# Kernel tuning notes

Hardware: AMD Instinct MI355X
Metric: run time of the kernel (lower is better)

The kernel has to match this reference:

```python
import jax, jax.numpy as jnp
import numpy as np

EPS = 1e-5

def _conv1x1(x, w, b):
    # x: [B,C,H,W], w: [O,C,1,1], b: [O]
    return jnp.einsum('oc,bchw->bohw', w[:, :, 0, 0], x) + b[None, :, None, None]

def _maxpool(x, s):
    return jax.lax.reduce_window(x, -jnp.inf, jax.lax.max,
                                 (1, 1, s, s), (1, 1, s, s), 'VALID')

def _sra(x, gw, gb, tw, tb, pw, pb, ww, wb, scale):
    # embedded-Gaussian non-local block with spatial sub-sampling on phi/g
    B, C, H, W = x.shape
    ic = gw.shape[0]
    g = _maxpool(_conv1x1(x, gw, gb), scale).reshape(B, ic, -1)    # [B,ic,n]
    phi = _maxpool(_conv1x1(x, pw, pb), scale).reshape(B, ic, -1)  # [B,ic,n]
    theta = _conv1x1(x, tw, tb).reshape(B, ic, -1)                 # [B,ic,N]
    f = jnp.einsum('bcn,bcm->bnm', theta, phi)                     # [B,N,n]
    a = jax.nn.softmax(f, axis=-1)
    y = jnp.einsum('bnm,bcm->bcn', a, g).reshape(B, ic, H, W)
    return _conv1x1(y, ww, wb) + x

def _conv_bn(x, w, gamma, beta, mean, var):
    y = jax.lax.conv_general_dilated(x, w, (1, 1), ((1, 1), (1, 1)),
                                     dimension_numbers=('NCHW', 'OIHW', 'NCHW'))
    inv = gamma / jnp.sqrt(var + EPS)
    return y * inv[None, :, None, None] + (beta - mean * inv)[None, :, None, None]

def setup_inputs() -> dict:
    key = jax.random.key(0)
    B, C = 4, 32
    sizes = [96, 48, 24]
    inp = {}
    ks = iter(jax.random.split(key, 64))
    for i, hw in enumerate(sizes):
        inp[f'fea1_{i}'] = jax.random.normal(next(ks), (B, C, hw, hw), jnp.float32)
        inp[f'fea2_{i}'] = jax.random.normal(next(ks), (B, C, hw, hw), jnp.float32)
    for lv in (1, 2, 3):
        for nm in ('g', 't', 'p'):
            inp[f'{nm}{lv}_w'] = jax.random.normal(next(ks), (C, 2 * C, 1, 1), jnp.float32) * 0.05
            inp[f'{nm}{lv}_b'] = jax.random.normal(next(ks), (C,), jnp.float32) * 0.05
        inp[f'w{lv}_w'] = jax.random.normal(next(ks), (2 * C, C, 1, 1), jnp.float32) * 0.05
        inp[f'w{lv}_b'] = jax.random.normal(next(ks), (2 * C,), jnp.float32) * 0.05
        inp[f'c{lv}_w'] = jax.random.normal(next(ks), (C, 2 * C, 3, 3), jnp.float32) * 0.05
        inp[f'bn{lv}_g'] = jax.random.uniform(next(ks), (C,), jnp.float32, 0.5, 1.5)
        inp[f'bn{lv}_b'] = jax.random.normal(next(ks), (C,), jnp.float32) * 0.05
        inp[f'bn{lv}_m'] = jax.random.normal(next(ks), (C,), jnp.float32) * 0.05
        inp[f'bn{lv}_v'] = jax.random.uniform(next(ks), (C,), jnp.float32, 0.5, 1.5)
    return inp

def reference(fea1_0, fea1_1, fea1_2, fea2_0, fea2_1, fea2_2,
              g1_w, g1_b, t1_w, t1_b, p1_w, p1_b, w1_w, w1_b, c1_w, bn1_g, bn1_b, bn1_m, bn1_v,
              g2_w, g2_b, t2_w, t2_b, p2_w, p2_b, w2_w, w2_b, c2_w, bn2_g, bn2_b, bn2_m, bn2_v,
              g3_w, g3_b, t3_w, t3_b, p3_w, p3_b, w3_w, w3_b, c3_w, bn3_g, bn3_b, bn3_m, bn3_v):
    x1 = jnp.concatenate([fea1_0, fea2_0], axis=1)
    x2 = jnp.concatenate([fea1_1, fea2_1], axis=1)
    x3 = jnp.concatenate([fea1_2, fea2_2], axis=1)
    z1 = _sra(x1, g1_w, g1_b, t1_w, t1_b, p1_w, p1_b, w1_w, w1_b, 2)
    z2 = _sra(x2, g2_w, g2_b, t2_w, t2_b, p2_w, p2_b, w2_w, w2_b, 4)
    z3 = _sra(x3, g3_w, g3_b, t3_w, t3_b, p3_w, p3_b, w3_w, w3_b, 8)
    out1 = _conv_bn(z1, c1_w, bn1_g, bn1_b, bn1_m, bn1_v)
    out2 = _conv_bn(z2, c2_w, bn2_g, bn2_b, bn2_m, bn2_v)
    out3 = _conv_bn(z3, c3_w, bn3_g, bn3_b, bn3_m, bn3_v)
    return (out1, out2, out3)
```

## Files before the change

kernel.cpp:

```cpp
#include <hip/hip_runtime.h>
#include <hip/hip_bf16.h>

typedef __hip_bfloat16 bf16;
typedef __attribute__((ext_vector_type(8))) short short8;
typedef __attribute__((ext_vector_type(4))) float floatx4;

__device__ __forceinline__ float b2f(bf16 v) { return __bfloat162float(v); }
__device__ __forceinline__ bf16 f2b(float v) { return __float2bfloat16(v); }
__device__ __forceinline__ float ldv(const void* p, size_t i, bool f32) {
    return f32 ? ((const float*)p)[i] : b2f(((const bf16*)p)[i]);
}
__device__ __forceinline__ float s2f(short s) {
    unsigned int u = ((unsigned int)(unsigned short)s) << 16;
    float f; __builtin_memcpy(&f, &u, 4); return f;
}
__device__ __forceinline__ short f2s(float f) {
    bf16 h = f2b(f); short s; __builtin_memcpy(&s, &h, 2); return s;
}
#define MFMA16(a, b, c) __builtin_amdgcn_mfma_f32_16x16x32_bf16(a, b, c, 0, 0, 0)

struct Ptrs { const void* p[45]; };

struct Lvl {
    const void *f1, *f2;
    const float *wtgp, *btgp, *wbf, *bfold;
    const bf16 *Wt, *Wc3;
    bf16 *th, *g, *p, *phi, *gt, *yp, *z;
    float* lp;
    int N, n, npad, split, W, s, wp, H, tX, BN;
    size_t outOff;
};

__global__ void k_detect(const void* x, int* flag) {
    __shared__ int cnt;
    if (threadIdx.x == 0) cnt = 0;
    __syncthreads();
    const unsigned short* us = (const unsigned short*)x;
    int local = 0;
    for (int i = threadIdx.x; i < 8192; i += 256) {
        unsigned e = us[2 * i] & 0x7F80u;
        if (e == 0x7F80u || e == 0u) local++;
    }
    atomicAdd(&cnt, local);
    __syncthreads();
    if (threadIdx.x == 0) flag[0] = (cnt >= 8) ? 1 : 0;
}

#define O_WTGP  0
#define O_BTGP  6144
#define O_WBF   6240
#define O_BFOLD 6304
#define O_WT    6336
#define O_WC3   7360
#define LVS     16576

__global__ void k_prep(Ptrs in, const int* flag, float* __restrict__ wsf)
{
    int lv = blockIdx.y;
    float* base = wsf + (size_t)lv * LVS;
    const int wb0 = 6 + 13 * lv;
    const void* gw  = in.p[wb0 + 0];
    const void* gb  = in.p[wb0 + 1];
    const void* tw  = in.p[wb0 + 2];
    const void* tb  = in.p[wb0 + 3];
    const void* pw  = in.p[wb0 + 4];
    const void* pb  = in.p[wb0 + 5];
    const void* ww  = in.p[wb0 + 6];
    const void* wb  = in.p[wb0 + 7];
    const void* cw  = in.p[wb0 + 8];
    const void* bng = in.p[wb0 + 9];
    const void* bnb = in.p[wb0 + 10];
    const void* bnm = in.p[wb0 + 11];
    const void* bnv = in.p[wb0 + 12];
    bool f32 = flag[0] != 0;
    int gid = blockIdx.x * 256 + threadIdx.x;
    int stride = gridDim.x * 256;

    float* wtgp = base + O_WTGP;
    float* btgp = base + O_BTGP;
    float* wbf = base + O_WBF;
    float* bfold = base + O_BFOLD;
    bf16* Wt = (bf16*)(base + O_WT);
    bf16* Wc3 = (bf16*)(base + O_WC3);

    for (int e = gid; e < 64 * 96; e += stride) {
        int k = e / 96, c = e % 96;
        float v;
        if (c < 32)      v = ldv(tw, (size_t)c * 64 + k, f32);
        else if (c < 64) v = ldv(gw, (size_t)(c - 32) * 64 + k, f32);
        else             v = ldv(pw, (size_t)(c - 64) * 64 + k, f32);
        wtgp[e] = v;
    }
    for (int e = gid; e < 96; e += stride) {
        float v = (e < 32) ? ldv(tb, e, f32)
                           : (e < 64 ? ldv(gb, e - 32, f32) : ldv(pb, e - 64, f32));
        btgp[e] = v;
    }
    for (int e = gid; e < 64 * 32; e += stride)
        Wt[e] = f2b(ldv(ww, e, f32));
    for (int e = gid; e < 64; e += stride) wbf[e] = ldv(wb, e, f32);
    for (int e = gid; e < 18432; e += stride) {
        int k = e & 31, n = (e >> 5) & 15, ot = (e >> 9) & 1;
        int tap = (e >> 10) % 9, cc = e / 9216;
        int o = ot * 16 + n, c = cc * 32 + k;
        float inv = ldv(bng, o, f32) * rsqrtf(ldv(bnv, o, f32) + 1e-5f);
        Wc3[e] = f2b(ldv(cw, ((size_t)o * 64 + c) * 9 + tap, f32) * inv);
    }
    for (int e = gid; e < 32; e += stride) {
        float inv = ldv(bng, e, f32) * rsqrtf(ldv(bnv, e, f32) + 1e-5f);
        bfold[e] = ldv(bnb, e, f32) - ldv(bnm, e, f32) * inv;
    }
}

__global__ void k_tgp(Lvl a0, Lvl a1, Lvl a2, int s1, int s2, const int* flag)
{
    bool f32 = flag[0] != 0;
    int bid = blockIdx.x;
    const Lvl P = bid < s1 ? a0 : (bid < s2 ? a1 : a2);
    int local = bid - (bid < s1 ? 0 : (bid < s2 ? s1 : s2));
    int nbp = P.BN >> 8;
    int grp = local / nbp;
    int pb = local - grp * nbp;
    bf16* dst = (grp == 0) ? P.th : ((grp == 1) ? P.g : P.p);
    int co = grp * 32;
    int gid = pb * 256 + threadIdx.x;
    int N = P.N;
    int b = gid / N;
    int ii = gid - b * N;
    float acc[32];
#pragma unroll
    for (int c = 0; c < 32; c++) acc[c] = P.btgp[co + c];
    size_t base = (size_t)b * 32 * N + ii;
    for (int k = 0; k < 32; k++) {
        float xv = ldv(P.f1, base + (size_t)k * N, f32);
        const float* w = P.wtgp + k * 96 + co;
#pragma unroll
        for (int c = 0; c < 32; c++) acc[c] += xv * w[c];
    }
    for (int k = 0; k < 32; k++) {
        float xv = ldv(P.f2, base + (size_t)k * N, f32);
        const float* w = P.wtgp + (k + 32) * 96 + co;
#pragma unroll
        for (int c = 0; c < 32; c++) acc[c] += xv * w[c];
    }
    bf16* dp = dst + (size_t)gid * 32;
#pragma unroll
    for (int c = 0; c < 32; c++) dp[c] = f2b(acc[c]);
}

__global__ void k_pool(Lvl a0, Lvl a1, Lvl a2, int s1, int s2)
{
    int bid = blockIdx.x;
    const Lvl P = bid < s1 ? a0 : (bid < s2 ? a1 : a2);
    int local = bid - (bid < s1 ? 0 : (bid < s2 ? s1 : s2));
    int gid = local * 256 + threadIdx.x;
    int npad = P.npad;
    if (gid >= 4 * npad * 32) return;
    int c = gid & 31;
    int j = (gid >> 5) % npad;
    int b = gid / (32 * npad);
    float mg = 0.f, mp = 0.f;
    if (j < P.n) {
        int py = j / P.wp, px = j - py * P.wp;
        const int N = P.N;
        mg = -INFINITY; mp = -INFINITY;
        for (int dy = 0; dy < P.s; dy++)
            for (int dx = 0; dx < P.s; dx++) {
                int idx = (py * P.s + dy) * P.W + px * P.s + dx;
                size_t bse = ((size_t)b * N + idx) * 32 + c;
                mg = fmaxf(mg, b2f(P.g[bse]));
                mp = fmaxf(mp, b2f(P.p[bse]));
            }
    }
    P.phi[((size_t)b * npad + j) * 32 + c] = f2b(mp);
    P.gt[((size_t)b * 32 + c) * npad + j] = f2b(mg);
}

__launch_bounds__(256)
__global__ void k_attn(Lvl a0, Lvl a1, Lvl a2, int s1, int s2)
{
    __shared__ __align__(16) bf16 Pt_s[4 * 1152];
    int bid = blockIdx.x;
    const Lvl P = bid < s1 ? a0 : (bid < s2 ? a1 : a2);
    int local = bid - (bid < s1 ? 0 : (bid < s2 ? s1 : s2));
    int rowblocks = P.BN >> 6;
    int c = local / rowblocks;
    int rb = local - c * rowblocks;

    int tid = threadIdx.x, lane = tid & 63, wv = tid >> 6;
    int quad = lane >> 4, col = lane & 15;
    bf16* Pt = Pt_s + wv * 1152;
    int row0 = rb * 64;
    int b = row0 / P.N;
    int npad = P.npad;

    short8 ta = *(const short8*)(P.th + (size_t)(row0 + wv * 16 + col) * 32 + quad * 8);
    const bf16* php = P.phi + (size_t)b * npad * 32 + (size_t)col * 32 + quad * 8;
    const bf16* gtp = P.gt + (size_t)b * 32 * npad + (size_t)col * npad + quad * 8;

    floatx4 y0 = {0.f, 0.f, 0.f, 0.f}, y1 = {0.f, 0.f, 0.f, 0.f};
    float lp4[4] = {0.f, 0.f, 0.f, 0.f};
    const floatx4 zc = {0.f, 0.f, 0.f, 0.f};

    int js = c ? P.split : 0;
    int je = c ? npad : P.split;
    for (int j0 = js; j0 < je; j0 += 64) {
        floatx4 s0 = MFMA16(ta, *(const short8*)(php + (size_t)(j0 +  0) * 32), zc);
        floatx4 s1 = MFMA16(ta, *(const short8*)(php + (size_t)(j0 + 16) * 32), zc);
        floatx4 s2 = MFMA16(ta, *(const short8*)(php + (size_t)(j0 + 32) * 32), zc);
        floatx4 s3 = MFMA16(ta, *(const short8*)(php + (size_t)(j0 + 48) * 32), zc);
#pragma unroll
        for (int r = 0; r < 4; r++) {
            float p0 = __expf(s0[r]), p1 = __expf(s1[r]);
            float p2 = __expf(s2[r]), p3 = __expf(s3[r]);
            lp4[r] += (p0 + p1) + (p2 + p3);
            bf16* pr = Pt + (quad * 4 + r) * 72;
            pr[ 0 + col] = f2b(p0);
            pr[16 + col] = f2b(p1);
            pr[32 + col] = f2b(p2);
            pr[48 + col] = f2b(p3);
        }
#pragma unroll
        for (int kc = 0; kc < 2; kc++) {
            short8 pa = *(const short8*)(Pt + col * 72 + kc * 32 + quad * 8);
            short8 g0 = *(const short8*)(gtp + j0 + kc * 32);
            short8 g1 = *(const short8*)(gtp + (size_t)16 * npad + j0 + kc * 32);
            y0 = MFMA16(pa, g0, y0);
            y1 = MFMA16(pa, g1, y1);
        }
    }

#pragma unroll
    for (int r = 0; r < 4; r++) {
        float v = lp4[r];
        v += __shfl_xor(v, 1); v += __shfl_xor(v, 2);
        v += __shfl_xor(v, 4); v += __shfl_xor(v, 8);
        int grow = row0 + wv * 16 + quad * 4 + r;
        size_t o = ((size_t)c * P.BN + grow) * 32;
        P.yp[o + col] = f2b(y0[r]);
        P.yp[o + 16 + col] = f2b(y1[r]);
        if (col == 0) P.lp[(size_t)c * P.BN + grow] = v;
    }
}

__launch_bounds__(256)
__global__ void k_merge(Lvl a0, Lvl a1, Lvl a2, int s1, int s2, const int* flag)
{
    bool f32 = flag[0] != 0;
    __shared__ __align__(16) float zb[64 * 65];
    int bid = blockIdx.x;
    const Lvl P = bid < s1 ? a0 : (bid < s2 ? a1 : a2);
    int rb = bid - (bid < s1 ? 0 : (bid < s2 ? s1 : s2));
    int tid = threadIdx.x, lane = tid & 63, wv = tid >> 6;
    int quad = lane >> 4, col = lane & 15;
    int row0 = rb * 64;
    int b = row0 / P.N;
    int pix0 = row0 - b * P.N;

    int grow = row0 + wv * 16 + col;
    short8 v0 = *(const short8*)(P.yp + (size_t)grow * 32 + quad * 8);
    short8 v1 = *(const short8*)(P.yp + ((size_t)P.BN + grow) * 32 + quad * 8);
    float L = P.lp[grow] + P.lp[(size_t)P.BN + grow] - (float)(P.npad - P.n);
    float invL = 1.f / L;
    short8 ya;
#pragma unroll
    for (int j = 0; j < 8; j++)
        ya[j] = f2s((s2f(v0[j]) + s2f(v1[j])) * invL);

    const floatx4 zc = {0.f, 0.f, 0.f, 0.f};
    floatx4 zt[4];
#pragma unroll
    for (int ot = 0; ot < 4; ot++) {
        short8 wbv = *(const short8*)(P.Wt + (size_t)(ot * 16 + col) * 32 + quad * 8);
        zt[ot] = MFMA16(ya, wbv, zc);
    }
#pragma unroll
    for (int ot = 0; ot < 4; ot++)
#pragma unroll
        for (int r = 0; r < 4; r++)
            zb[(wv * 16 + quad * 4 + r) * 65 + ot * 16 + col] = zt[ot][r];
    __syncthreads();

    const void* fx = (wv < 2) ? P.f1 : P.f2;
#pragma unroll
    for (int k = 0; k < 16; k++) {
        int o = wv * 16 + k, op = o & 31;
        float a = zb[lane * 65 + o] + P.wbf[o];
        a += ldv(fx, (size_t)(b * 32 + op) * P.N + pix0 + lane, f32);
        P.z[((size_t)(b * 64 + o)) * P.N + pix0 + lane] = f2b(a);
    }
}

__launch_bounds__(256)
__global__ void k_conv3m(Lvl a0, Lvl a1, Lvl a2, int s1, int s2,
                         void* out, const int* flag)
{
    bool f32 = flag[0] != 0;
    __shared__ __align__(16) bf16 zh[324 * 34];
    int bid = blockIdx.x;
    const Lvl P = bid < s1 ? a0 : (bid < s2 ? a1 : a2);
    int local = bid - (bid < s1 ? 0 : (bid < s2 ? s1 : s2));
    const int H = P.H, W = H, Npix = H * W, tX = P.tX;
    int tid = threadIdx.x, lane = tid & 63, wv = tid >> 6;
    int quad = lane >> 4, col = lane & 15;
    int tpi = tX * tX;
    int b = local / tpi;
    int t = local - b * tpi;
    int ty = t / tX, tx = t - ty * tX;
    int y0 = ty * 16, x0 = tx * 16;

    floatx4 acc[4][2];
#pragma unroll
    for (int pt = 0; pt < 4; pt++)
#pragma unroll
        for (int ot = 0; ot < 2; ot++) acc[pt][ot] = (floatx4){0.f, 0.f, 0.f, 0.f};

    for (int cc = 0; cc < 2; cc++) {
        __syncthreads();
        for (int e = tid; e < 324 * 32; e += 256) {
            int c = e / 324, pix = e - c * 324;
            int hy = pix / 18, hx = pix - hy * 18;
            int gy = y0 - 1 + hy, gx = x0 - 1 + hx;
            bf16 v = f2b(0.f);
            if (gy >= 0 && gy < H && gx >= 0 && gx < W)
                v = P.z[((size_t)(b * 64 + cc * 32 + c)) * Npix + gy * W + gx];
            zh[pix * 34 + c] = v;
        }
        __syncthreads();
        short8 Bf[9][2];
        const bf16* wp = P.Wc3 + (size_t)cc * 9216 + col * 32 + quad * 8;
#pragma unroll
        for (int tap = 0; tap < 9; tap++)
#pragma unroll
            for (int ot = 0; ot < 2; ot++)
                Bf[tap][ot] = *(const short8*)(wp + (tap * 2 + ot) * 512);
#pragma unroll
        for (int pt = 0; pt < 4; pt++) {
            int yy = wv * 4 + pt;
#pragma unroll
            for (int tap = 0; tap < 9; tap++) {
                int dy = tap / 3, dx = tap - dy * 3;
                short8 A = *(const short8*)(zh + ((yy + dy) * 18 + (col + dx)) * 34 + quad * 8);
                acc[pt][0] = MFMA16(A, Bf[tap][0], acc[pt][0]);
                acc[pt][1] = MFMA16(A, Bf[tap][1], acc[pt][1]);
            }
        }
    }
#pragma unroll
    for (int pt = 0; pt < 4; pt++) {
        int oy = y0 + wv * 4 + pt;
        if (oy >= H) continue;
#pragma unroll
        for (int ot = 0; ot < 2; ot++) {
            int o = ot * 16 + col;
            size_t ob = P.outOff + (size_t)(b * 32 + o) * Npix + (size_t)oy * W;
            float bias = P.bfold[o];
#pragma unroll
            for (int r = 0; r < 4; r++) {
                int ox = x0 + quad * 4 + r;
                if (ox >= W) continue;
                float a = acc[pt][ot][r] + bias;
                if (f32) ((float*)out)[ob + ox] = a;
                else     ((bf16*)out)[ob + ox] = f2b(a);
            }
        }
    }
}

extern "C" void kernel_launch(void* const* d_in, const int* in_sizes, int n_in,
                              void* d_out, int out_size, void* d_ws, size_t ws_size,
                              hipStream_t stream)
{
    const int Hs[3] = {96, 48, 24};
    const int ss[3] = {2, 4, 8};
    const int npads[3] = {2304, 192, 64};
    const int splits[3] = {1152, 128, 64};
    const size_t outOff[3] = {0, 1179648, 1474560};

    int* flag = (int*)d_ws;
    float* wsf = (float*)d_ws + 16;
    float* lpbase = wsf + 3 * LVS;
    bf16* bb = (bf16*)(lpbase + 96768);

    const size_t o_gp[3] = {0, 2359296, 2949120};
    const size_t R_TH = 3096576;
    const size_t o_th[3] = {R_TH, R_TH + 1179648, R_TH + 1474560};
    const size_t R_PHI = 4644864;
    const size_t o_phi[3] = {R_PHI, R_PHI + 294912, R_PHI + 319488};
    const size_t R_GT = 4972544;
    const size_t o_gt[3] = {R_GT, R_GT + 294912, R_GT + 319488};
    const size_t o_z[3] = {R_TH, R_TH + 2359296, R_TH + 2949120};
    const size_t o_lp[3] = {0, 73728, 92160};

    k_detect<<<1, 256, 0, stream>>>(d_in[0], flag);

    Ptrs hp;
    for (int i = 0; i < 45 && i < n_in; i++) hp.p[i] = d_in[i];
    k_prep<<<dim3(8, 3), 256, 0, stream>>>(hp, flag, wsf);

    Lvl L[3];
    for (int lv = 0; lv < 3; lv++) {
        int H = Hs[lv], N = H * H;
        float* base = wsf + (size_t)lv * LVS;
        L[lv].f1 = d_in[2 * lv];
        L[lv].f2 = d_in[2 * lv + 1];
        L[lv].wtgp = base + O_WTGP;
        L[lv].btgp = base + O_BTGP;
        L[lv].wbf = base + O_WBF;
        L[lv].bfold = base + O_BFOLD;
        L[lv].Wt = (const bf16*)(base + O_WT);
        L[lv].Wc3 = (const bf16*)(base + O_WC3);
        L[lv].th = bb + o_th[lv];
        L[lv].g = bb + o_gp[lv];
        L[lv].p = bb + o_gp[lv] + (size_t)4 * N * 32;
        L[lv].phi = bb + o_phi[lv];
        L[lv].gt = bb + o_gt[lv];
        L[lv].yp = bb + o_gp[lv];
        L[lv].z = bb + o_z[lv];
        L[lv].lp = lpbase + o_lp[lv];
        L[lv].N = N;
        L[lv].n = (H / ss[lv]) * (H / ss[lv]);
        L[lv].npad = npads[lv];
        L[lv].split = splits[lv];
        L[lv].W = H;
        L[lv].s = ss[lv];
        L[lv].wp = H / ss[lv];
        L[lv].H = H;
        L[lv].tX = (H + 15) / 16;
        L[lv].BN = 4 * N;
        L[lv].outOff = outOff[lv];
    }

    k_tgp<<<567, 256, 0, stream>>>(L[0], L[1], L[2], 432, 540, flag);
    k_pool<<<1280, 256, 0, stream>>>(L[0], L[1], L[2], 1152, 1248);
    k_attn<<<1512, 256, 0, stream>>>(L[0], L[1], L[2], 1152, 1440);
    k_merge<<<756, 256, 0, stream>>>(L[0], L[1], L[2], 576, 720, flag);
    k_conv3m<<<196, 256, 0, stream>>>(L[0], L[1], L[2], 144, 180, d_out, flag);
}
```

Baseline: 320.0 us.

## Generalize attention key split to configurable chunks with register prefetch and double-buffered LDS

Replaces the fixed two-way split of the softmax key dimension with a per-level chunk count (up to four for the largest level when the workspace is large enough), launching more attention blocks. The merge kernel sums the partial numerators and denominators across all chunks. Inside the attention loop, the phi and g tiles for the next iteration are prefetched into registers and the P tile alternates between two LDS buffers to overlap loads with MFMA work. The workspace layout is reorganised to hold the larger partial buffers, at the cost of more LDS, more registers per thread and more partial-result traffic.

```diff
diff --git a/kernel.cpp b/kernel.cpp
--- a/kernel.cpp
+++ b/kernel.cpp
@@ -27,7 +27,7 @@
     const bf16 *Wt, *Wc3;
     bf16 *th, *g, *p, *phi, *gt, *yp, *z;
     float* lp;
-    int N, n, npad, split, W, s, wp, H, tX, BN;
+    int N, n, npad, nch, W, s, wp, H, tX, BN;
     size_t outOff;
 };
 
@@ -179,7 +179,7 @@
 __launch_bounds__(256)
 __global__ void k_attn(Lvl a0, Lvl a1, Lvl a2, int s1, int s2)
 {
-    __shared__ __align__(16) bf16 Pt_s[4 * 1152];
+    __shared__ __align__(16) bf16 Pt_s[8 * 1152];
     int bid = blockIdx.x;
     const Lvl P = bid < s1 ? a0 : (bid < s2 ? a1 : a2);
     int local = bid - (bid < s1 ? 0 : (bid < s2 ? s1 : s2));
@@ -189,11 +189,15 @@
 
     int tid = threadIdx.x, lane = tid & 63, wv = tid >> 6;
     int quad = lane >> 4, col = lane & 15;
-    bf16* Pt = Pt_s + wv * 1152;
+    bf16* Pt0 = Pt_s + wv * 2304;
     int row0 = rb * 64;
     int b = row0 / P.N;
     int npad = P.npad;
 
+    int T = npad >> 6, C = P.nch;
+    int js = ((T * c) / C) << 6;
+    int je = ((T * (c + 1)) / C) << 6;
+
     short8 ta = *(const short8*)(P.th + (size_t)(row0 + wv * 16 + col) * 32 + quad * 8);
     const bf16* php = P.phi + (size_t)b * npad * 32 + (size_t)col * 32 + quad * 8;
     const bf16* gtp = P.gt + (size_t)b * 32 * npad + (size_t)col * npad + quad * 8;
@@ -202,19 +206,37 @@
     float lp4[4] = {0.f, 0.f, 0.f, 0.f};
     const floatx4 zc = {0.f, 0.f, 0.f, 0.f};
 
-    int js = c ? P.split : 0;
-    int je = c ? npad : P.split;
+    short8 ph[4], gg[4];
+#pragma unroll
+    for (int k = 0; k < 4; k++)
+        ph[k] = *(const short8*)(php + (size_t)(js + 16 * k) * 32);
+    gg[0] = *(const short8*)(gtp + js);
+    gg[1] = *(const short8*)(gtp + js + 32);
+    gg[2] = *(const short8*)(gtp + (size_t)16 * npad + js);
+    gg[3] = *(const short8*)(gtp + (size_t)16 * npad + js + 32);
+
     for (int j0 = js; j0 < je; j0 += 64) {
-        floatx4 s0 = MFMA16(ta, *(const short8*)(php + (size_t)(j0 +  0) * 32), zc);
-        floatx4 s1 = MFMA16(ta, *(const short8*)(php + (size_t)(j0 + 16) * 32), zc);
-        floatx4 s2 = MFMA16(ta, *(const short8*)(php + (size_t)(j0 + 32) * 32), zc);
-        floatx4 s3 = MFMA16(ta, *(const short8*)(php + (size_t)(j0 + 48) * 32), zc);
+        int jn = (j0 + 64 < je) ? j0 + 64 : js;
+        short8 phN[4], ggN[4];
+#pragma unroll
+        for (int k = 0; k < 4; k++)
+            phN[k] = *(const short8*)(php + (size_t)(jn + 16 * k) * 32);
+        ggN[0] = *(const short8*)(gtp + jn);
+        ggN[1] = *(const short8*)(gtp + jn + 32);
+        ggN[2] = *(const short8*)(gtp + (size_t)16 * npad + jn);
+        ggN[3] = *(const short8*)(gtp + (size_t)16 * npad + jn + 32);
+
+        floatx4 s0 = MFMA16(ta, ph[0], zc);
+        floatx4 s1 = MFMA16(ta, ph[1], zc);
+        floatx4 s2 = MFMA16(ta, ph[2], zc);
+        floatx4 s3 = MFMA16(ta, ph[3], zc);
+        bf16* PtW = Pt0 + (((j0 - js) & 64) ? 1152 : 0);
 #pragma unroll
         for (int r = 0; r < 4; r++) {
             float p0 = __expf(s0[r]), p1 = __expf(s1[r]);
             float p2 = __expf(s2[r]), p3 = __expf(s3[r]);
             lp4[r] += (p0 + p1) + (p2 + p3);
-            bf16* pr = Pt + (quad * 4 + r) * 72;
+            bf16* pr = PtW + (quad * 4 + r) * 72;
             pr[ 0 + col] = f2b(p0);
             pr[16 + col] = f2b(p1);
             pr[32 + col] = f2b(p2);
@@ -222,12 +244,12 @@
         }
 #pragma unroll
         for (int kc = 0; kc < 2; kc++) {
-            short8 pa = *(const short8*)(Pt + col * 72 + kc * 32 + quad * 8);
-            short8 g0 = *(const short8*)(gtp + j0 + kc * 32);
-            short8 g1 = *(const short8*)(gtp + (size_t)16 * npad + j0 + kc * 32);
-            y0 = MFMA16(pa, g0, y0);
-            y1 = MFMA16(pa, g1, y1);
+            short8 pa = *(const short8*)(PtW + col * 72 + kc * 32 + quad * 8);
+            y0 = MFMA16(pa, gg[kc], y0);
+            y1 = MFMA16(pa, gg[2 + kc], y1);
         }
+#pragma unroll
+        for (int k = 0; k < 4; k++) { ph[k] = phN[k]; gg[k] = ggN[k]; }
     }
 
 #pragma unroll
@@ -258,14 +280,18 @@
     int pix0 = row0 - b * P.N;
 
     int grow = row0 + wv * 16 + col;
-    short8 v0 = *(const short8*)(P.yp + (size_t)grow * 32 + quad * 8);
-    short8 v1 = *(const short8*)(P.yp + ((size_t)P.BN + grow) * 32 + quad * 8);
-    float L = P.lp[grow] + P.lp[(size_t)P.BN + grow] - (float)(P.npad - P.n);
+    float yv[8] = {0.f, 0.f, 0.f, 0.f, 0.f, 0.f, 0.f, 0.f};
+    float L = -(float)(P.npad - P.n);
+    for (int cc = 0; cc < P.nch; cc++) {
+        short8 v = *(const short8*)(P.yp + ((size_t)cc * P.BN + grow) * 32 + quad * 8);
+#pragma unroll
+        for (int j = 0; j < 8; j++) yv[j] += s2f(v[j]);
+        L += P.lp[(size_t)cc * P.BN + grow];
+    }
     float invL = 1.f / L;
     short8 ya;
 #pragma unroll
-    for (int j = 0; j < 8; j++)
-        ya[j] = f2s((s2f(v0[j]) + s2f(v1[j])) * invL);
+    for (int j = 0; j < 8; j++) ya[j] = f2s(yv[j] * invL);
 
     const floatx4 zc = {0.f, 0.f, 0.f, 0.f};
     floatx4 zt[4];
@@ -374,23 +400,27 @@
     const int Hs[3] = {96, 48, 24};
     const int ss[3] = {2, 4, 8};
     const int npads[3] = {2304, 192, 64};
-    const int splits[3] = {1152, 128, 64};
     const size_t outOff[3] = {0, 1179648, 1474560};
+    const int BNs[3] = {36864, 9216, 2304};
+
+    bool hi = ws_size >= 18600000ULL;
+    int nch[3]; nch[0] = hi ? 4 : 2; nch[1] = hi ? 3 : 2; nch[2] = 1;
 
     int* flag = (int*)d_ws;
     float* wsf = (float*)d_ws + 16;
     float* lpbase = wsf + 3 * LVS;
-    bf16* bb = (bf16*)(lpbase + 96768);
-
-    const size_t o_gp[3] = {0, 2359296, 2949120};
-    const size_t R_TH = 3096576;
-    const size_t o_th[3] = {R_TH, R_TH + 1179648, R_TH + 1474560};
-    const size_t R_PHI = 4644864;
-    const size_t o_phi[3] = {R_PHI, R_PHI + 294912, R_PHI + 319488};
-    const size_t R_GT = 4972544;
-    const size_t o_gt[3] = {R_GT, R_GT + 294912, R_GT + 319488};
-    const size_t o_z[3] = {R_TH, R_TH + 2359296, R_TH + 2949120};
-    const size_t o_lp[3] = {0, 73728, 92160};
+    size_t lpo[3], lpacc = 0;
+    for (int lv = 0; lv < 3; lv++) { lpo[lv] = lpacc; lpacc += (size_t)nch[lv] * BNs[lv]; }
+    bf16* bb = (bf16*)(lpbase + lpacc);
+
+    const size_t gpo[3] = {0, 2359296, 2949120};
+    size_t ypo[3], ypacc = 0;
+    for (int lv = 0; lv < 3; lv++) { ypo[lv] = ypacc; ypacc += (size_t)nch[lv] * BNs[lv] * 32; }
+    size_t Asz = ypacc > 3096576 ? ypacc : 3096576;
+    const size_t tho[3] = {0, 1179648, 1474560};
+    const size_t pho[3] = {1548288, 2138112, 2187264};
+    const size_t gto[3] = {1843200, 2162688, 2195456};
+    const size_t zo[3]  = {0, 2359296, 2949120};
 
     k_detect<<<1, 256, 0, stream>>>(d_in[0], flag);
 
@@ -410,18 +440,18 @@
         L[lv].bfold = base + O_BFOLD;
         L[lv].Wt = (const bf16*)(base + O_WT);
         L[lv].Wc3 = (const bf16*)(base + O_WC3);
-        L[lv].th = bb + o_th[lv];
-        L[lv].g = bb + o_gp[lv];
-        L[lv].p = bb + o_gp[lv] + (size_t)4 * N * 32;
-        L[lv].phi = bb + o_phi[lv];
-        L[lv].gt = bb + o_gt[lv];
-        L[lv].yp = bb + o_gp[lv];
-        L[lv].z = bb + o_z[lv];
-        L[lv].lp = lpbase + o_lp[lv];
+        L[lv].g = bb + gpo[lv];
+        L[lv].p = bb + gpo[lv] + (size_t)4 * N * 32;
+        L[lv].yp = bb + ypo[lv];
+        L[lv].th = bb + Asz + tho[lv];
+        L[lv].phi = bb + Asz + pho[lv];
+        L[lv].gt = bb + Asz + gto[lv];
+        L[lv].z = bb + Asz + zo[lv];
+        L[lv].lp = lpbase + lpo[lv];
         L[lv].N = N;
         L[lv].n = (H / ss[lv]) * (H / ss[lv]);
         L[lv].npad = npads[lv];
-        L[lv].split = splits[lv];
+        L[lv].nch = nch[lv];
         L[lv].W = H;
         L[lv].s = ss[lv];
         L[lv].wp = H / ss[lv];
@@ -431,9 +461,10 @@
         L[lv].outOff = outOff[lv];
     }
 
+    int a0 = nch[0] * (BNs[0] >> 6), a1 = nch[1] * (BNs[1] >> 6), a2 = nch[2] * (BNs[2] >> 6);
     k_tgp<<<567, 256, 0, stream>>>(L[0], L[1], L[2], 432, 540, flag);
     k_pool<<<1280, 256, 0, stream>>>(L[0], L[1], L[2], 1152, 1248);
-    k_attn<<<1512, 256, 0, stream>>>(L[0], L[1], L[2], 1152, 1440);
+    k_attn<<<a0 + a1 + a2, 256, 0, stream>>>(L[0], L[1], L[2], a0, a0 + a1);
     k_merge<<<756, 256, 0, stream>>>(L[0], L[1], L[2], 576, 720, flag);
     k_conv3m<<<196, 256, 0, stream>>>(L[0], L[1], L[2], 144, 180, d_out, flag);
 }
```

After: 323.0 us. About the same (+0.9%).
